# Kernel optimization log

Hardware: AMD Instinct MI355X
Metric: run time of the kernel (lower is better)

## Reference

```python
import jax, jax.numpy as jnp
import numpy as np

N_NODES = 100000
DEG = 16
N_EDGES = N_NODES * DEG
D_FEAT = 64
HIDDEN = 64
K_RATIO = 0.5  # self.k
EPS = 1e-08


@jax.custom_vjp
def binary_step(x):
    return (x > 0.0).astype(x.dtype)

def _bs_fwd(x):
    return binary_step(x), x

def _bs_bwd(x, g):
    ax = jnp.abs(x)
    # BinaryStep surrogate gradient: 0 for |x|>1, 0.4 for 0.4<|x|<=1, else 2-4|x|
    add = jnp.where(ax > 1.0, 0.0, jnp.where(ax > 0.4, 0.4, 2.0 - 4.0 * ax))
    return (g * add,)

binary_step.defvjp(_bs_fwd, _bs_bwd)


def segment_softmax(v, seg, n):
    # torch.sparse.softmax(dim=1) == softmax over edges grouped by row id
    m = jax.ops.segment_max(v, seg, num_segments=n)
    e = jnp.exp(v - m[seg])
    s = jax.ops.segment_sum(e, seg, num_segments=n)
    return e / s[seg]


def setup_inputs() -> dict:
    key = jax.random.key(0)
    k1, k2, k3, k4, k5, k6, k7 = jax.random.split(key, 7)
    # coalesced edge list: rows sorted, (row,col) unique, every node has DEG edges
    rows = np.repeat(np.arange(N_NODES, dtype=np.int32), DEG)
    offs = np.tile(np.arange(1, DEG + 1, dtype=np.int32), N_NODES)
    cols = ((rows + offs) % N_NODES).reshape(N_NODES, DEG)
    cols = np.sort(cols, axis=1).reshape(-1).astype(np.int32)
    indices = jnp.asarray(np.stack([rows, cols]))  # [2, E]
    features = jax.random.normal(k1, (N_NODES, D_FEAT), dtype=jnp.float32)
    values = jax.random.uniform(k2, (N_EDGES,), dtype=jnp.float32, minval=0.1, maxval=1.0)
    U = jax.random.uniform(k3, (N_EDGES,), dtype=jnp.float32)
    gumbel = -jnp.log(-jnp.log(U + EPS) + EPS)  # Gumbel(0,1) noise (precomputed for determinism)
    in_dim = 2 * D_FEAT + 1
    w0 = jax.random.normal(k4, (HIDDEN, in_dim), dtype=jnp.float32) * (6.0 / (in_dim + HIDDEN)) ** 0.5
    b0 = jax.random.normal(k5, (HIDDEN,), dtype=jnp.float32) * 0.02
    w1 = jax.random.normal(k6, (1, HIDDEN), dtype=jnp.float32) * (6.0 / (HIDDEN + 1)) ** 0.5
    b1 = jax.random.normal(k7, (1,), dtype=jnp.float32) * 0.02
    return {"features": features, "values": values, "w0": w0, "b0": b0,
            "w1": w1, "b1": b1, "gumbel": gumbel, "indices": indices,
            "n_nodes": N_NODES, "temperature": 1}


def reference(features, values, w0, b0, w1, b1, gumbel, indices, n_nodes, temperature):
    rows = indices[0]
    cols = indices[1]
    # gather endpoint features + edge weight, 2-layer MLP -> scalar score per edge
    temp = jnp.concatenate([features[rows], features[cols], values[:, None]], axis=-1)  # [E, 2D+1]
    h = jax.nn.relu(temp @ w0.T + b0)          # [E, H]
    z = (h @ w1.T + b1).reshape(-1)            # [E]
    z = z / jnp.maximum(jnp.linalg.norm(z), 1e-12)  # F.normalize(dim=0)
    pi = segment_softmax(z, rows, n_nodes)           # sparse row softmax
    logits = (jnp.log(pi) + gumbel) / temperature    # gumbel_softmax_sample (training path)
    y = segment_softmax(logits, rows, n_nodes)
    # per-node top-k threshold masking
    counts = jax.ops.segment_sum(jnp.ones_like(rows), rows, num_segments=n_nodes)  # [N]
    k_edges = jnp.maximum(jnp.round(counts.astype(y.dtype) * K_RATIO).astype(rows.dtype), 1)
    val_sort_idx = jnp.argsort(-y)                                   # global descending sort
    idx_sort_idx = jnp.argsort(rows[val_sort_idx], stable=True)      # stable regroup by row
    scores_sorted = y[val_sort_idx][idx_sort_idx]                    # per-row descending scores
    rows_sorted = rows[val_sort_idx][idx_sort_idx]
    edge_start = jnp.concatenate([jnp.zeros((1,), counts.dtype), jnp.cumsum(counts[:-1])])
    edge_end = jnp.abs(edge_start + k_edges - 1)
    node_thre = scores_sorted[edge_end]          # k-th largest score per node
    thre_aug = node_thre[rows_sorted]            # == repeat_interleave(counts) since rows_sorted ascending
    mask = binary_step(scores_sorted - thre_aug + 1e-12)
    masked = mask * scores_sorted
    masked = masked[jnp.argsort(idx_sort_idx)]   # undo row regroup
    masked = masked[jnp.argsort(val_sort_idx)]   # undo value sort -> original edge order
    return masked
```

## Files before the change

### kernel.cpp

```cpp
#include <hip/hip_runtime.h>

#define N_NODES 100000
#define DEG 16
#define N_EDGES (N_NODES * DEG)
#define NT 64
#define NBLK2 ((N_NODES + NT - 1) / NT)

__global__ __launch_bounds__(256) void k_ab(const float* __restrict__ feat,
                                            const float* __restrict__ w0,
                                            const float* __restrict__ b0,
                                            float* __restrict__ AB) {
    __shared__ float ws[64][128];
    __shared__ float fs[64][64];
    const int tid = threadIdx.x;

    for (int idx = tid; idx < 64 * 128; idx += 256) {
        int k = idx >> 7, o = idx & 127;
        ws[k][o] = (o < 64) ? w0[o * 129 + k] : w0[(o - 64) * 129 + 64 + k];
    }
    const int n0 = blockIdx.x * 64;
    for (int idx = tid; idx < 1024; idx += 256) {
        int flat = idx << 2;
        int nn = flat >> 6, k = flat & 63;
        int n = n0 + nn;
        float4 v = make_float4(0.f, 0.f, 0.f, 0.f);
        if (n < N_NODES) v = *(const float4*)(feat + (size_t)n * 64 + k);
        *(float4*)&fs[nn][k] = v;
    }
    __syncthreads();

    const int to = tid & 31;
    const int tn = tid >> 5;
    float acc[8][4];
#pragma unroll
    for (int a = 0; a < 8; ++a) {
        acc[a][0] = 0.f; acc[a][1] = 0.f; acc[a][2] = 0.f; acc[a][3] = 0.f;
    }
#pragma unroll 2
    for (int k = 0; k < 64; k += 4) {
        float4 w40 = *(const float4*)&ws[k + 0][to * 4];
        float4 w41 = *(const float4*)&ws[k + 1][to * 4];
        float4 w42 = *(const float4*)&ws[k + 2][to * 4];
        float4 w43 = *(const float4*)&ws[k + 3][to * 4];
#pragma unroll
        for (int a = 0; a < 8; ++a) {
            float4 f4 = *(const float4*)&fs[tn * 8 + a][k];
            acc[a][0] = fmaf(f4.x, w40.x, acc[a][0]);
            acc[a][1] = fmaf(f4.x, w40.y, acc[a][1]);
            acc[a][2] = fmaf(f4.x, w40.z, acc[a][2]);
            acc[a][3] = fmaf(f4.x, w40.w, acc[a][3]);
            acc[a][0] = fmaf(f4.y, w41.x, acc[a][0]);
            acc[a][1] = fmaf(f4.y, w41.y, acc[a][1]);
            acc[a][2] = fmaf(f4.y, w41.z, acc[a][2]);
            acc[a][3] = fmaf(f4.y, w41.w, acc[a][3]);
            acc[a][0] = fmaf(f4.z, w42.x, acc[a][0]);
            acc[a][1] = fmaf(f4.z, w42.y, acc[a][1]);
            acc[a][2] = fmaf(f4.z, w42.z, acc[a][2]);
            acc[a][3] = fmaf(f4.z, w42.w, acc[a][3]);
            acc[a][0] = fmaf(f4.w, w43.x, acc[a][0]);
            acc[a][1] = fmaf(f4.w, w43.y, acc[a][1]);
            acc[a][2] = fmaf(f4.w, w43.z, acc[a][2]);
            acc[a][3] = fmaf(f4.w, w43.w, acc[a][3]);
        }
    }
    float4 bb = make_float4(0.f, 0.f, 0.f, 0.f);
    if (to < 16) bb = *(const float4*)(b0 + to * 4);
#pragma unroll
    for (int a = 0; a < 8; ++a) {
        int n = n0 + tn * 8 + a;
        if (n < N_NODES) {
            float4 o4 = make_float4(acc[a][0] + bb.x, acc[a][1] + bb.y,
                                    acc[a][2] + bb.z, acc[a][3] + bb.w);
            *(float4*)(AB + (size_t)n * 128 + to * 4) = o4;
        }
    }
}

__global__ __launch_bounds__(256) void k_edge(const float* __restrict__ AB,
                                              const float* __restrict__ values,
                                              const int* __restrict__ indices,
                                              const float* __restrict__ w0,
                                              const float* __restrict__ w1,
                                              const float* __restrict__ b1,
                                              float* __restrict__ z,
                                              double* __restrict__ partial) {
    __shared__ float a_s[64][68];
    __shared__ float b_s[80][68];
    __shared__ float wv_s[64];
    __shared__ float w1_s[64];
    __shared__ double red[256];
    const int t = threadIdx.x;
    const int n0 = blockIdx.x * NT;
    const int nvalid = min(NT, N_NODES - n0);

    if (t < 64) {
        wv_s[t] = w0[t * 129 + 128];
        w1_s[t] = w1[t];
    }
    for (int idx = t; idx < 1024; idx += 256) {
        int r = idx >> 4, k4 = idx & 15;
        float4 v = make_float4(0.f, 0.f, 0.f, 0.f);
        if (r < nvalid) v = *(const float4*)(AB + (size_t)(n0 + r) * 128 + k4 * 4);
        *(float4*)&a_s[r][k4 * 4] = v;
    }
    for (int idx = t; idx < 1280; idx += 256) {
        int r = idx >> 4, k4 = idx & 15;
        int node = n0 + 1 + r;
        if (node >= N_NODES) node -= N_NODES;
        *(float4*)&b_s[r][k4 * 4] = *(const float4*)(AB + (size_t)node * 128 + 64 + k4 * 4);
    }
    __syncthreads();

    const int row = t >> 2;
    const bool ok = row < nvalid;
    double ss = 0.0;
    if (ok) {
        const int ebase = n0 * 16 + (t << 2);
        int4   c4 = *(const int4*)(indices + N_EDGES + ebase);
        float4 v4 = *(const float4*)(values + ebase);
        int   cols[4] = {c4.x, c4.y, c4.z, c4.w};
        float vv[4]   = {v4.x, v4.y, v4.z, v4.w};
        int   ii[4];
        bool  fb[4];
        bool  anyfb = false;
#pragma unroll
        for (int k = 0; k < 4; ++k) {
            int i = cols[k] - (n0 + 1);
            if (i < 0) i += N_NODES;
            fb[k] = (i >= 80);
            anyfb |= fb[k];
            ii[k] = fb[k] ? 0 : i;
        }
        float acc[4] = {0.f, 0.f, 0.f, 0.f};
#pragma unroll
        for (int q = 0; q < 16; ++q) {
            float4 a4  = *(const float4*)&a_s[row][q * 4];
            float4 wv4 = *(const float4*)&wv_s[q * 4];
            float4 w14 = *(const float4*)&w1_s[q * 4];
#pragma unroll
            for (int k = 0; k < 4; ++k) {
                float4 b4 = *(const float4*)&b_s[ii[k]][q * 4];
                float t0 = fmaf(wv4.x, vv[k], a4.x + b4.x);
                float t1 = fmaf(wv4.y, vv[k], a4.y + b4.y);
                float t2 = fmaf(wv4.z, vv[k], a4.z + b4.z);
                float t3 = fmaf(wv4.w, vv[k], a4.w + b4.w);
                acc[k] = fmaf(w14.x, fmaxf(t0, 0.f), acc[k]);
                acc[k] = fmaf(w14.y, fmaxf(t1, 0.f), acc[k]);
                acc[k] = fmaf(w14.z, fmaxf(t2, 0.f), acc[k]);
                acc[k] = fmaf(w14.w, fmaxf(t3, 0.f), acc[k]);
            }
        }
        if (anyfb) {
#pragma unroll
            for (int k = 0; k < 4; ++k) {
                if (fb[k]) {
                    const float* Bp = AB + (size_t)cols[k] * 128 + 64;
                    float a = 0.f;
                    for (int h = 0; h < 64; ++h) {
                        float th = fmaf(wv_s[h], vv[k], a_s[row][h] + Bp[h]);
                        a = fmaf(w1_s[h], fmaxf(th, 0.f), a);
                    }
                    acc[k] = a;
                }
            }
        }
        const float b1v = b1[0];
        float4 z4;
        z4.x = acc[0] + b1v; z4.y = acc[1] + b1v;
        z4.z = acc[2] + b1v; z4.w = acc[3] + b1v;
        *(float4*)(z + ebase) = z4;
        ss = (double)z4.x * z4.x + (double)z4.y * z4.y +
             (double)z4.z * z4.z + (double)z4.w * z4.w;
    }
    red[t] = ss;
    __syncthreads();
#pragma unroll
    for (int off = 128; off > 0; off >>= 1) {
        if (t < off) red[t] += red[t + off];
        __syncthreads();
    }
    if (t == 0) partial[blockIdx.x] = red[0];
}

__global__ __launch_bounds__(256) void k_norm(const double* __restrict__ partial,
                                              double* __restrict__ nrm) {
    __shared__ double red[256];
    const int t = threadIdx.x;
    double s = 0.0;
    for (int i = t; i < NBLK2; i += 256) s += partial[i];
    red[t] = s;
    __syncthreads();
#pragma unroll
    for (int off = 128; off > 0; off >>= 1) {
        if (t < off) red[t] += red[t + off];
        __syncthreads();
    }
    if (t == 0) nrm[0] = fmax(sqrt(red[0]), 1e-12);
}

__global__ __launch_bounds__(256) void k_mask(const float* __restrict__ z,
                                              const float* __restrict__ gumbel,
                                              const double* __restrict__ nrm,
                                              const int* __restrict__ temperature,
                                              float* __restrict__ out) {
    const int n = blockIdx.x * 256 + threadIdx.x;
    if (n >= N_NODES) return;
    const double inv_nv = 1.0 / nrm[0];
    const double invT = 1.0 / (double)temperature[0];
    const float4* z4 = (const float4*)(z + (size_t)n * 16);
    const float4* g4 = (const float4*)(gumbel + (size_t)n * 16);
    double tl[16], y[16];
#pragma unroll
    for (int q = 0; q < 4; ++q) {
        float4 zv = z4[q];
        float4 gv = g4[q];
        tl[q * 4 + 0] = ((double)zv.x * inv_nv + (double)gv.x) * invT;
        tl[q * 4 + 1] = ((double)zv.y * inv_nv + (double)gv.y) * invT;
        tl[q * 4 + 2] = ((double)zv.z * inv_nv + (double)gv.z) * invT;
        tl[q * 4 + 3] = ((double)zv.w * inv_nv + (double)gv.w) * invT;
    }
    double m = tl[0];
#pragma unroll
    for (int i = 1; i < 16; ++i) m = fmax(m, tl[i]);
    double s = 0.0;
#pragma unroll
    for (int i = 0; i < 16; ++i) { y[i] = exp(tl[i] - m); s += y[i]; }
    const double inv_s = 1.0 / s;
#pragma unroll
    for (int i = 0; i < 16; ++i) y[i] *= inv_s;
    double thre = y[0];
#pragma unroll
    for (int i = 0; i < 16; ++i) {
        int c = 0, q = 0;
#pragma unroll
        for (int j = 0; j < 16; ++j) {
            c += (y[j] > y[i]) ? 1 : 0;
            q += (y[j] == y[i]) ? 1 : 0;
        }
        if (c <= 7 && 7 < c + q) thre = y[i];
    }
    float4* o4 = (float4*)(out + (size_t)n * 16);
#pragma unroll
    for (int qq = 0; qq < 4; ++qq) {
        float4 ov;
        ov.x = ((y[qq * 4 + 0] - thre + 1e-12) > 0.0) ? (float)y[qq * 4 + 0] : 0.f;
        ov.y = ((y[qq * 4 + 1] - thre + 1e-12) > 0.0) ? (float)y[qq * 4 + 1] : 0.f;
        ov.z = ((y[qq * 4 + 2] - thre + 1e-12) > 0.0) ? (float)y[qq * 4 + 2] : 0.f;
        ov.w = ((y[qq * 4 + 3] - thre + 1e-12) > 0.0) ? (float)y[qq * 4 + 3] : 0.f;
        o4[qq] = ov;
    }
}

extern "C" void kernel_launch(void* const* d_in, const int* in_sizes, int n_in,
                              void* d_out, int out_size, void* d_ws, size_t ws_size,
                              hipStream_t stream) {
    const float* feat    = (const float*)d_in[0];
    const float* values  = (const float*)d_in[1];
    const float* w0      = (const float*)d_in[2];
    const float* b0      = (const float*)d_in[3];
    const float* w1      = (const float*)d_in[4];
    const float* b1      = (const float*)d_in[5];
    const float* gumbel  = (const float*)d_in[6];
    const int*   indices = (const int*)d_in[7];
    const int*   temp    = (const int*)d_in[9];
    float* out = (float*)d_out;

    float*  AB      = (float*)d_ws;
    float*  zbuf    = (float*)((char*)d_ws + (size_t)N_NODES * 128 * 4);
    double* partial = (double*)((char*)d_ws + (size_t)N_NODES * 128 * 4 + (size_t)N_EDGES * 4);
    double* nrm     = partial + NBLK2;

    k_ab  <<<(N_NODES + 63) / 64, 256, 0, stream>>>(feat, w0, b0, AB);
    k_edge<<<NBLK2, 256, 0, stream>>>(AB, values, indices, w0, w1, b1, zbuf, partial);
    k_norm<<<1, 256, 0, stream>>>(partial, nrm);
    k_mask<<<(N_NODES + 255) / 256, 256, 0, stream>>>(zbuf, gumbel, nrm, temp, out);
}
```

Before: 78.78 us.

## Fuse per-node projection GEMM into edge kernel, drop AB intermediate buffer

Merges the per-node linear projection (k_ab) into the edge-scoring kernel. Each block now computes the A-half for its 64 nodes and the B-half for an 81-node halo directly from features held in shared memory, using a transposed weight copy prepared once by a tiny kernel. This removes the write and re-read of the 100000x128 AB workspace and one kernel launch. In exchange the B projection is recomputed for the overlapping halo rows, shared memory is reused across phases with extra barriers, and the rare out-of-window fallback path now recomputes a 64x64 dot product per edge.

```diff
diff --git a/kernel.cpp b/kernel.cpp
--- a/kernel.cpp
+++ b/kernel.cpp
@@ -6,115 +6,176 @@
 #define NT 64
 #define NBLK2 ((N_NODES + NT - 1) / NT)
 
-__global__ __launch_bounds__(256) void k_ab(const float* __restrict__ feat,
-                                            const float* __restrict__ w0,
-                                            const float* __restrict__ b0,
-                                            float* __restrict__ AB) {
-    __shared__ float ws[64][128];
-    __shared__ float fs[64][64];
-    const int tid = threadIdx.x;
-
-    for (int idx = tid; idx < 64 * 128; idx += 256) {
-        int k = idx >> 7, o = idx & 127;
-        ws[k][o] = (o < 64) ? w0[o * 129 + k] : w0[(o - 64) * 129 + 64 + k];
-    }
-    const int n0 = blockIdx.x * 64;
-    for (int idx = tid; idx < 1024; idx += 256) {
-        int flat = idx << 2;
-        int nn = flat >> 6, k = flat & 63;
-        int n = n0 + nn;
-        float4 v = make_float4(0.f, 0.f, 0.f, 0.f);
-        if (n < N_NODES) v = *(const float4*)(feat + (size_t)n * 64 + k);
-        *(float4*)&fs[nn][k] = v;
-    }
-    __syncthreads();
-
-    const int to = tid & 31;
-    const int tn = tid >> 5;
-    float acc[8][4];
-#pragma unroll
-    for (int a = 0; a < 8; ++a) {
-        acc[a][0] = 0.f; acc[a][1] = 0.f; acc[a][2] = 0.f; acc[a][3] = 0.f;
-    }
-#pragma unroll 2
-    for (int k = 0; k < 64; k += 4) {
-        float4 w40 = *(const float4*)&ws[k + 0][to * 4];
-        float4 w41 = *(const float4*)&ws[k + 1][to * 4];
-        float4 w42 = *(const float4*)&ws[k + 2][to * 4];
-        float4 w43 = *(const float4*)&ws[k + 3][to * 4];
-#pragma unroll
-        for (int a = 0; a < 8; ++a) {
-            float4 f4 = *(const float4*)&fs[tn * 8 + a][k];
-            acc[a][0] = fmaf(f4.x, w40.x, acc[a][0]);
-            acc[a][1] = fmaf(f4.x, w40.y, acc[a][1]);
-            acc[a][2] = fmaf(f4.x, w40.z, acc[a][2]);
-            acc[a][3] = fmaf(f4.x, w40.w, acc[a][3]);
-            acc[a][0] = fmaf(f4.y, w41.x, acc[a][0]);
-            acc[a][1] = fmaf(f4.y, w41.y, acc[a][1]);
-            acc[a][2] = fmaf(f4.y, w41.z, acc[a][2]);
-            acc[a][3] = fmaf(f4.y, w41.w, acc[a][3]);
-            acc[a][0] = fmaf(f4.z, w42.x, acc[a][0]);
-            acc[a][1] = fmaf(f4.z, w42.y, acc[a][1]);
-            acc[a][2] = fmaf(f4.z, w42.z, acc[a][2]);
-            acc[a][3] = fmaf(f4.z, w42.w, acc[a][3]);
-            acc[a][0] = fmaf(f4.w, w43.x, acc[a][0]);
-            acc[a][1] = fmaf(f4.w, w43.y, acc[a][1]);
-            acc[a][2] = fmaf(f4.w, w43.z, acc[a][2]);
-            acc[a][3] = fmaf(f4.w, w43.w, acc[a][3]);
-        }
-    }
-    float4 bb = make_float4(0.f, 0.f, 0.f, 0.f);
-    if (to < 16) bb = *(const float4*)(b0 + to * 4);
-#pragma unroll
-    for (int a = 0; a < 8; ++a) {
-        int n = n0 + tn * 8 + a;
-        if (n < N_NODES) {
-            float4 o4 = make_float4(acc[a][0] + bb.x, acc[a][1] + bb.y,
-                                    acc[a][2] + bb.z, acc[a][3] + bb.w);
-            *(float4*)(AB + (size_t)n * 128 + to * 4) = o4;
-        }
-    }
-}
-
-__global__ __launch_bounds__(256) void k_edge(const float* __restrict__ AB,
-                                              const float* __restrict__ values,
-                                              const int* __restrict__ indices,
-                                              const float* __restrict__ w0,
-                                              const float* __restrict__ w1,
-                                              const float* __restrict__ b1,
-                                              float* __restrict__ z,
-                                              double* __restrict__ partial) {
-    __shared__ float a_s[64][68];
-    __shared__ float b_s[80][68];
-    __shared__ float wv_s[64];
-    __shared__ float w1_s[64];
-    __shared__ double red[256];
-    const int t = threadIdx.x;
+#define FS 68
+#define OFF_FEAT 0
+#define OFF_WS   5508
+#define OFF_BS   7556
+#define OFF_WV   12996
+#define OFF_W1   13060
+#define OFF_B0   13124
+#define SM_TOT   13188
+
+__global__ __launch_bounds__(256) void k_prep(const float* __restrict__ w0,
+                                              float* __restrict__ w0T) {
+    int id = blockIdx.x * 256 + threadIdx.x;
+    if (id < 64 * 128) {
+        int k = id >> 7, o = id & 127;
+        w0T[k * 128 + o] = (o < 64) ? w0[o * 129 + k]
+                                    : w0[(o - 64) * 129 + 64 + k];
+    }
+}
+
+__global__ __launch_bounds__(256) void k_fused(const float* __restrict__ feat,
+                                               const float* __restrict__ values,
+                                               const int* __restrict__ indices,
+                                               const float* __restrict__ w0,
+                                               const float* __restrict__ w0T,
+                                               const float* __restrict__ b0,
+                                               const float* __restrict__ w1,
+                                               const float* __restrict__ b1,
+                                               float* __restrict__ z,
+                                               double* __restrict__ partial) {
+    __shared__ float smem[SM_TOT];
+    float* fs   = smem + OFF_FEAT;
+    float* wsm  = smem + OFF_WS;
+    float* bsm  = smem + OFF_BS;
+    float* a_s  = smem + OFF_FEAT;
+    float* wv_s = smem + OFF_WV;
+    float* w1_s = smem + OFF_W1;
+    float* b0_s = smem + OFF_B0;
+
+    const int t  = threadIdx.x;
     const int n0 = blockIdx.x * NT;
     const int nvalid = min(NT, N_NODES - n0);
 
     if (t < 64) {
         wv_s[t] = w0[t * 129 + 128];
         w1_s[t] = w1[t];
-    }
-    for (int idx = t; idx < 1024; idx += 256) {
+        b0_s[t] = b0[t];
+    }
+    for (int idx = t; idx < 81 * 16; idx += 256) {
         int r = idx >> 4, k4 = idx & 15;
-        float4 v = make_float4(0.f, 0.f, 0.f, 0.f);
-        if (r < nvalid) v = *(const float4*)(AB + (size_t)(n0 + r) * 128 + k4 * 4);
-        *(float4*)&a_s[r][k4 * 4] = v;
-    }
-    for (int idx = t; idx < 1280; idx += 256) {
-        int r = idx >> 4, k4 = idx & 15;
-        int node = n0 + 1 + r;
+        int node = n0 + r;
         if (node >= N_NODES) node -= N_NODES;
-        *(float4*)&b_s[r][k4 * 4] = *(const float4*)(AB + (size_t)node * 128 + 64 + k4 * 4);
+        *(float4*)&fs[r * FS + k4 * 4] =
+            *(const float4*)&feat[(size_t)node * 64 + k4 * 4];
+    }
+    for (int idx = t; idx < 512; idx += 256) {
+        int k = idx >> 4, o4 = idx & 15;
+        *(float4*)&wsm[k * 64 + o4 * 4] =
+            *(const float4*)&w0T[k * 128 + 64 + o4 * 4];
+    }
+    __syncthreads();
+
+    const int to = t & 15;
+    const int tn = t >> 4;
+
+#define FMA16(ACCR, F4)                                   \
+    ACCR[0] = fmaf(F4.x, w40.x, ACCR[0]);                 \
+    ACCR[1] = fmaf(F4.x, w40.y, ACCR[1]);                 \
+    ACCR[2] = fmaf(F4.x, w40.z, ACCR[2]);                 \
+    ACCR[3] = fmaf(F4.x, w40.w, ACCR[3]);                 \
+    ACCR[0] = fmaf(F4.y, w41.x, ACCR[0]);                 \
+    ACCR[1] = fmaf(F4.y, w41.y, ACCR[1]);                 \
+    ACCR[2] = fmaf(F4.y, w41.z, ACCR[2]);                 \
+    ACCR[3] = fmaf(F4.y, w41.w, ACCR[3]);                 \
+    ACCR[0] = fmaf(F4.z, w42.x, ACCR[0]);                 \
+    ACCR[1] = fmaf(F4.z, w42.y, ACCR[1]);                 \
+    ACCR[2] = fmaf(F4.z, w42.z, ACCR[2]);                 \
+    ACCR[3] = fmaf(F4.z, w42.w, ACCR[3]);                 \
+    ACCR[0] = fmaf(F4.w, w43.x, ACCR[0]);                 \
+    ACCR[1] = fmaf(F4.w, w43.y, ACCR[1]);                 \
+    ACCR[2] = fmaf(F4.w, w43.z, ACCR[2]);                 \
+    ACCR[3] = fmaf(F4.w, w43.w, ACCR[3]);
+
+    float accB[5][4];
+#pragma unroll
+    for (int rr = 0; rr < 5; ++rr) {
+        accB[rr][0] = 0.f; accB[rr][1] = 0.f; accB[rr][2] = 0.f; accB[rr][3] = 0.f;
+    }
+#pragma unroll 1
+    for (int h = 0; h < 2; ++h) {
+        if (h == 1) {
+            __syncthreads();
+            for (int idx = t; idx < 512; idx += 256) {
+                int k = idx >> 4, o4 = idx & 15;
+                *(float4*)&wsm[k * 64 + o4 * 4] =
+                    *(const float4*)&w0T[(32 + k) * 128 + 64 + o4 * 4];
+            }
+            __syncthreads();
+        }
+#pragma unroll
+        for (int k4 = 0; k4 < 8; ++k4) {
+            const int kk = k4 * 4;
+            float4 w40 = *(const float4*)&wsm[(kk + 0) * 64 + to * 4];
+            float4 w41 = *(const float4*)&wsm[(kk + 1) * 64 + to * 4];
+            float4 w42 = *(const float4*)&wsm[(kk + 2) * 64 + to * 4];
+            float4 w43 = *(const float4*)&wsm[(kk + 3) * 64 + to * 4];
+#pragma unroll
+            for (int rr = 0; rr < 5; ++rr) {
+                float4 f4 = *(const float4*)&fs[(tn * 5 + rr + 1) * FS + h * 32 + kk];
+                FMA16(accB[rr], f4)
+            }
+        }
+    }
+    __syncthreads();
+#pragma unroll
+    for (int rr = 0; rr < 5; ++rr) {
+        float4 o4v = make_float4(accB[rr][0], accB[rr][1], accB[rr][2], accB[rr][3]);
+        *(float4*)&bsm[(tn * 5 + rr) * FS + to * 4] = o4v;
+    }
+    for (int idx = t; idx < 512; idx += 256) {
+        int k = idx >> 4, o4 = idx & 15;
+        *(float4*)&wsm[k * 64 + o4 * 4] =
+            *(const float4*)&w0T[k * 128 + o4 * 4];
+    }
+    __syncthreads();
+
+    float accA[4][4];
+#pragma unroll
+    for (int rr = 0; rr < 4; ++rr) {
+        accA[rr][0] = 0.f; accA[rr][1] = 0.f; accA[rr][2] = 0.f; accA[rr][3] = 0.f;
+    }
+#pragma unroll 1
+    for (int h = 0; h < 2; ++h) {
+        if (h == 1) {
+            __syncthreads();
+            for (int idx = t; idx < 512; idx += 256) {
+                int k = idx >> 4, o4 = idx & 15;
+                *(float4*)&wsm[k * 64 + o4 * 4] =
+                    *(const float4*)&w0T[(32 + k) * 128 + o4 * 4];
+            }
+            __syncthreads();
+        }
+#pragma unroll
+        for (int k4 = 0; k4 < 8; ++k4) {
+            const int kk = k4 * 4;
+            float4 w40 = *(const float4*)&wsm[(kk + 0) * 64 + to * 4];
+            float4 w41 = *(const float4*)&wsm[(kk + 1) * 64 + to * 4];
+            float4 w42 = *(const float4*)&wsm[(kk + 2) * 64 + to * 4];
+            float4 w43 = *(const float4*)&wsm[(kk + 3) * 64 + to * 4];
+#pragma unroll
+            for (int rr = 0; rr < 4; ++rr) {
+                float4 f4 = *(const float4*)&fs[(tn * 4 + rr) * FS + h * 32 + kk];
+                FMA16(accA[rr], f4)
+            }
+        }
+    }
+    __syncthreads();
+    {
+        float4 bb = *(const float4*)&b0_s[to * 4];
+#pragma unroll
+        for (int rr = 0; rr < 4; ++rr) {
+            float4 o4v = make_float4(accA[rr][0] + bb.x, accA[rr][1] + bb.y,
+                                     accA[rr][2] + bb.z, accA[rr][3] + bb.w);
+            *(float4*)&a_s[(tn * 4 + rr) * FS + to * 4] = o4v;
+        }
     }
     __syncthreads();
 
     const int row = t >> 2;
-    const bool ok = row < nvalid;
     double ss = 0.0;
-    if (ok) {
+    if (row < nvalid) {
         const int ebase = n0 * 16 + (t << 2);
         int4   c4 = *(const int4*)(indices + N_EDGES + ebase);
         float4 v4 = *(const float4*)(values + ebase);
@@ -134,12 +195,12 @@
         float acc[4] = {0.f, 0.f, 0.f, 0.f};
 #pragma unroll
         for (int q = 0; q < 16; ++q) {
-            float4 a4  = *(const float4*)&a_s[row][q * 4];
+            float4 a4  = *(const float4*)&a_s[row * FS + q * 4];
             float4 wv4 = *(const float4*)&wv_s[q * 4];
             float4 w14 = *(const float4*)&w1_s[q * 4];
 #pragma unroll
             for (int k = 0; k < 4; ++k) {
-                float4 b4 = *(const float4*)&b_s[ii[k]][q * 4];
+                float4 b4 = *(const float4*)&bsm[ii[k] * FS + q * 4];
                 float t0 = fmaf(wv4.x, vv[k], a4.x + b4.x);
                 float t1 = fmaf(wv4.y, vv[k], a4.y + b4.y);
                 float t2 = fmaf(wv4.z, vv[k], a4.z + b4.z);
@@ -151,14 +212,17 @@
             }
         }
         if (anyfb) {
-#pragma unroll
+#pragma unroll 1
             for (int k = 0; k < 4; ++k) {
                 if (fb[k]) {
-                    const float* Bp = AB + (size_t)cols[k] * 128 + 64;
+                    const float* fcol = feat + (size_t)cols[k] * 64;
                     float a = 0.f;
-                    for (int h = 0; h < 64; ++h) {
-                        float th = fmaf(wv_s[h], vv[k], a_s[row][h] + Bp[h]);
-                        a = fmaf(w1_s[h], fmaxf(th, 0.f), a);
+                    for (int hh = 0; hh < 64; ++hh) {
+                        float bh = 0.f;
+                        for (int kk2 = 0; kk2 < 64; ++kk2)
+                            bh = fmaf(fcol[kk2], w0T[kk2 * 128 + 64 + hh], bh);
+                        float th = fmaf(wv_s[hh], vv[k], a_s[row * FS + hh] + bh);
+                        a = fmaf(w1_s[hh], fmaxf(th, 0.f), a);
                     }
                     acc[k] = a;
                 }
@@ -172,6 +236,7 @@
         ss = (double)z4.x * z4.x + (double)z4.y * z4.y +
              (double)z4.z * z4.z + (double)z4.w * z4.w;
     }
+    double* red = (double*)(smem + OFF_WS);
     red[t] = ss;
     __syncthreads();
 #pragma unroll
@@ -265,13 +330,14 @@
     const int*   temp    = (const int*)d_in[9];
     float* out = (float*)d_out;
 
-    float*  AB      = (float*)d_ws;
-    float*  zbuf    = (float*)((char*)d_ws + (size_t)N_NODES * 128 * 4);
-    double* partial = (double*)((char*)d_ws + (size_t)N_NODES * 128 * 4 + (size_t)N_EDGES * 4);
+    float*  w0T     = (float*)d_ws;
+    float*  zbuf    = (float*)((char*)d_ws + 64 * 128 * 4);
+    double* partial = (double*)((char*)d_ws + 64 * 128 * 4 + (size_t)N_EDGES * 4);
     double* nrm     = partial + NBLK2;
 
-    k_ab  <<<(N_NODES + 63) / 64, 256, 0, stream>>>(feat, w0, b0, AB);
-    k_edge<<<NBLK2, 256, 0, stream>>>(AB, values, indices, w0, w1, b1, zbuf, partial);
-    k_norm<<<1, 256, 0, stream>>>(partial, nrm);
-    k_mask<<<(N_NODES + 255) / 256, 256, 0, stream>>>(zbuf, gumbel, nrm, temp, out);
-}
+    k_prep <<<32, 256, 0, stream>>>(w0, w0T);
+    k_fused<<<NBLK2, 256, 0, stream>>>(feat, values, indices, w0, w0T, b0, w1, b1,
+                                       zbuf, partial);
+    k_norm <<<1, 256, 0, stream>>>(partial, nrm);
+    k_mask <<<(N_NODES + 255) / 256, 256, 0, stream>>>(zbuf, gumbel, nrm, temp, out);
+}
```

New measurement: 111.3 us. 41.2% more time.

## Pre-transpose w0 in a prep kernel and halve k_ab weight shared memory

Applied to the files above, without the earlier changes.

Adds a small prep kernel that writes w0 once in a transposed, contiguous layout, so each k_ab block loads weights with coalesced float4 reads instead of a strided scalar gather. The weight tile in shared memory shrinks from 64 to 32 rows and is loaded in two halves, which lowers LDS use per block and may allow more blocks per CU. The cost is an extra kernel launch, an extra pair of block barriers in k_ab, and a shifted workspace layout.

```diff
diff --git a/kernel.cpp b/kernel.cpp
--- a/kernel.cpp
+++ b/kernel.cpp
@@ -6,19 +6,25 @@
 #define NT 64
 #define NBLK2 ((N_NODES + NT - 1) / NT)
 
+__global__ __launch_bounds__(256) void k_prep(const float* __restrict__ w0,
+                                              float* __restrict__ w0T) {
+    int id = blockIdx.x * 256 + threadIdx.x;
+    if (id < 64 * 128) {
+        int k = id >> 7, o = id & 127;
+        w0T[k * 128 + o] = (o < 64) ? w0[o * 129 + k]
+                                    : w0[(o - 64) * 129 + 64 + k];
+    }
+}
+
 __global__ __launch_bounds__(256) void k_ab(const float* __restrict__ feat,
-                                            const float* __restrict__ w0,
+                                            const float* __restrict__ w0T,
                                             const float* __restrict__ b0,
                                             float* __restrict__ AB) {
-    __shared__ float ws[64][128];
+    __shared__ float ws[32][128];
     __shared__ float fs[64][64];
     const int tid = threadIdx.x;
-
-    for (int idx = tid; idx < 64 * 128; idx += 256) {
-        int k = idx >> 7, o = idx & 127;
-        ws[k][o] = (o < 64) ? w0[o * 129 + k] : w0[(o - 64) * 129 + 64 + k];
-    }
     const int n0 = blockIdx.x * 64;
+
     for (int idx = tid; idx < 1024; idx += 256) {
         int flat = idx << 2;
         int nn = flat >> 6, k = flat & 63;
@@ -27,40 +33,61 @@
         if (n < N_NODES) v = *(const float4*)(feat + (size_t)n * 64 + k);
         *(float4*)&fs[nn][k] = v;
     }
+    for (int idx = tid; idx < 1024; idx += 256) {
+        int k = idx >> 5, o4 = idx & 31;
+        *(float4*)&ws[k][o4 * 4] = *(const float4*)&w0T[k * 128 + o4 * 4];
+    }
     __syncthreads();
 
     const int to = tid & 31;
     const int tn = tid >> 5;
+
+#define FMA16(ACCR, F4)                                   \
+    ACCR[0] = fmaf(F4.x, w40.x, ACCR[0]);                 \
+    ACCR[1] = fmaf(F4.x, w40.y, ACCR[1]);                 \
+    ACCR[2] = fmaf(F4.x, w40.z, ACCR[2]);                 \
+    ACCR[3] = fmaf(F4.x, w40.w, ACCR[3]);                 \
+    ACCR[0] = fmaf(F4.y, w41.x, ACCR[0]);                 \
+    ACCR[1] = fmaf(F4.y, w41.y, ACCR[1]);                 \
+    ACCR[2] = fmaf(F4.y, w41.z, ACCR[2]);                 \
+    ACCR[3] = fmaf(F4.y, w41.w, ACCR[3]);                 \
+    ACCR[0] = fmaf(F4.z, w42.x, ACCR[0]);                 \
+    ACCR[1] = fmaf(F4.z, w42.y, ACCR[1]);                 \
+    ACCR[2] = fmaf(F4.z, w42.z, ACCR[2]);                 \
+    ACCR[3] = fmaf(F4.z, w42.w, ACCR[3]);                 \
+    ACCR[0] = fmaf(F4.w, w43.x, ACCR[0]);                 \
+    ACCR[1] = fmaf(F4.w, w43.y, ACCR[1]);                 \
+    ACCR[2] = fmaf(F4.w, w43.z, ACCR[2]);                 \
+    ACCR[3] = fmaf(F4.w, w43.w, ACCR[3]);
+
     float acc[8][4];
 #pragma unroll
     for (int a = 0; a < 8; ++a) {
         acc[a][0] = 0.f; acc[a][1] = 0.f; acc[a][2] = 0.f; acc[a][3] = 0.f;
     }
-#pragma unroll 2
-    for (int k = 0; k < 64; k += 4) {
-        float4 w40 = *(const float4*)&ws[k + 0][to * 4];
-        float4 w41 = *(const float4*)&ws[k + 1][to * 4];
-        float4 w42 = *(const float4*)&ws[k + 2][to * 4];
-        float4 w43 = *(const float4*)&ws[k + 3][to * 4];
-#pragma unroll
-        for (int a = 0; a < 8; ++a) {
-            float4 f4 = *(const float4*)&fs[tn * 8 + a][k];
-            acc[a][0] = fmaf(f4.x, w40.x, acc[a][0]);
-            acc[a][1] = fmaf(f4.x, w40.y, acc[a][1]);
-            acc[a][2] = fmaf(f4.x, w40.z, acc[a][2]);
-            acc[a][3] = fmaf(f4.x, w40.w, acc[a][3]);
-            acc[a][0] = fmaf(f4.y, w41.x, acc[a][0]);
-            acc[a][1] = fmaf(f4.y, w41.y, acc[a][1]);
-            acc[a][2] = fmaf(f4.y, w41.z, acc[a][2]);
-            acc[a][3] = fmaf(f4.y, w41.w, acc[a][3]);
-            acc[a][0] = fmaf(f4.z, w42.x, acc[a][0]);
-            acc[a][1] = fmaf(f4.z, w42.y, acc[a][1]);
-            acc[a][2] = fmaf(f4.z, w42.z, acc[a][2]);
-            acc[a][3] = fmaf(f4.z, w42.w, acc[a][3]);
-            acc[a][0] = fmaf(f4.w, w43.x, acc[a][0]);
-            acc[a][1] = fmaf(f4.w, w43.y, acc[a][1]);
-            acc[a][2] = fmaf(f4.w, w43.z, acc[a][2]);
-            acc[a][3] = fmaf(f4.w, w43.w, acc[a][3]);
+#pragma unroll 1
+    for (int h = 0; h < 2; ++h) {
+        if (h == 1) {
+            __syncthreads();
+            for (int idx = tid; idx < 1024; idx += 256) {
+                int k = idx >> 5, o4 = idx & 31;
+                *(float4*)&ws[k][o4 * 4] =
+                    *(const float4*)&w0T[(32 + k) * 128 + o4 * 4];
+            }
+            __syncthreads();
+        }
+#pragma unroll
+        for (int k4 = 0; k4 < 8; ++k4) {
+            const int kk = k4 * 4;
+            float4 w40 = *(const float4*)&ws[kk + 0][to * 4];
+            float4 w41 = *(const float4*)&ws[kk + 1][to * 4];
+            float4 w42 = *(const float4*)&ws[kk + 2][to * 4];
+            float4 w43 = *(const float4*)&ws[kk + 3][to * 4];
+#pragma unroll
+            for (int a = 0; a < 8; ++a) {
+                float4 f4 = *(const float4*)&fs[tn * 8 + a][h * 32 + kk];
+                FMA16(acc[a], f4)
+            }
         }
     }
     float4 bb = make_float4(0.f, 0.f, 0.f, 0.f);
@@ -265,12 +292,15 @@
     const int*   temp    = (const int*)d_in[9];
     float* out = (float*)d_out;
 
-    float*  AB      = (float*)d_ws;
-    float*  zbuf    = (float*)((char*)d_ws + (size_t)N_NODES * 128 * 4);
-    double* partial = (double*)((char*)d_ws + (size_t)N_NODES * 128 * 4 + (size_t)N_EDGES * 4);
+    float*  w0T     = (float*)d_ws;
+    float*  AB      = (float*)((char*)d_ws + 64 * 128 * 4);
+    float*  zbuf    = (float*)((char*)d_ws + 64 * 128 * 4 + (size_t)N_NODES * 128 * 4);
+    double* partial = (double*)((char*)d_ws + 64 * 128 * 4 + (size_t)N_NODES * 128 * 4
+                                + (size_t)N_EDGES * 4);
     double* nrm     = partial + NBLK2;
 
-    k_ab  <<<(N_NODES + 63) / 64, 256, 0, stream>>>(feat, w0, b0, AB);
+    k_prep<<<32, 256, 0, stream>>>(w0, w0T);
+    k_ab  <<<(N_NODES + 63) / 64, 256, 0, stream>>>(feat, w0T, b0, AB);
     k_edge<<<NBLK2, 256, 0, stream>>>(AB, values, indices, w0, w1, b1, zbuf, partial);
     k_norm<<<1, 256, 0, stream>>>(partial, nrm);
     k_mask<<<(N_NODES + 255) / 256, 256, 0, stream>>>(zbuf, gumbel, nrm, temp, out);
```

Result: no change. 80.19 us (+1.8%).
